# Performance work log

Measured on AMD Instinct MI355X. Metric: run time of the kernel, lower is better.

The kernel has to match this reference:

```python
import jax, jax.numpy as jnp
import numpy as np
import math

B, C, P = 4, 256, 4096
H = 4
EPS = 1e-5


def setup_inputs() -> dict:
    key = jax.random.key(0)
    ks = jax.random.split(key, 6)
    s = 1.0 / math.sqrt(C)
    return {
        "x": jax.random.normal(ks[0], (B, C, P), jnp.float32),
        "wq": jax.random.normal(ks[1], (C, C), jnp.float32) * s,
        "wk": jax.random.normal(ks[2], (C, C), jnp.float32) * s,
        "wv": jax.random.normal(ks[3], (C, C), jnp.float32) * s,
        "wt": jax.random.normal(ks[4], (C, C), jnp.float32) * s,
        "bt": jax.random.normal(ks[5], (C,), jnp.float32) * 0.01,
        "gamma": jnp.ones((C,), jnp.float32),
        "beta": jnp.zeros((C,), jnp.float32),
    }


def reference(x, wq, wk, wv, wt, bt, gamma, beta):
    b, c, p = x.shape
    d = c // H  # head dim
    # 1x1 Conv1d == channel matmul: [C_out, C_in] @ [B, C_in, P]
    q = jnp.einsum("oc,bcp->bop", wq, x).reshape(b, H, d, p)
    k = jnp.einsum("oc,bcp->bop", wk, x).reshape(b, H, d, p)
    v = jnp.einsum("oc,bcp->bop", wv, x).reshape(b, H, d, p)
    # scores: x_q [b,h,p,d] @ x_k [b,h,d,p] -> [b,h,p,p]
    scores = jnp.einsum("bhdi,bhdj->bhij", q, k) / jnp.sqrt(jnp.float32(d))
    attn = jax.nn.softmax(scores, axis=-1)
    # attn @ v^T: [b,h,p,p] @ [b,h,p,d] -> [b,h,p,d], then back to [b,c,p]
    o = jnp.einsum("bhij,bhdj->bhdi", attn, v).reshape(b, c, p)
    # trans_conv(o - x) + bias
    y = jnp.einsum("oc,bcp->bop", wt, o - x) + bt[None, :, None]
    # BatchNorm1d (training mode): per-channel stats over (batch, points), biased var
    mean = jnp.mean(y, axis=(0, 2), keepdims=True)
    var = jnp.mean(jnp.square(y - mean), axis=(0, 2), keepdims=True)
    y = (y - mean) * jax.lax.rsqrt(var + EPS)
    y = y * gamma[None, :, None] + beta[None, :, None]
    return x + jax.nn.relu(y)
```

## Files before the change

kernel.cpp:

```cpp
#include <hip/hip_runtime.h>
#include <stdint.h>

#define B_ 4
#define C_ 256
#define P_ 4096
#define H_ 4
#define EPS_ 1e-5f
#define LOG2E 1.4426950408889634f

typedef __attribute__((ext_vector_type(8))) short short8v;
typedef __attribute__((ext_vector_type(4))) float floatx4;
#define MFMA16 __builtin_amdgcn_mfma_f32_16x16x32_bf16

#define GLOAD16(gp, lp)                                                     \
  __builtin_amdgcn_global_load_lds(                                         \
      (const __attribute__((address_space(1))) uint32_t*)(gp),              \
      (__attribute__((address_space(3))) uint32_t*)(lp), 16, 0, 0)

#define EXP2IP(x) asm("v_exp_f32 %0, %0" : "+v"(x))

__device__ __forceinline__ ushort f2bf(float f) {
  union { float f; uint32_t u; } c; c.f = f;
  uint32_t r = c.u + 0x7FFFu + ((c.u >> 16) & 1u);
  return (ushort)(r >> 16);
}
__device__ __forceinline__ float bf2f(ushort u) {
  union { uint32_t u; float f; } c; c.u = ((uint32_t)u) << 16; return c.f;
}

__global__ __launch_bounds__(256) void cast_kernel(
    const float* __restrict__ x, ushort* __restrict__ xb) {
  const int p0 = blockIdx.x * 64;
  const int c0 = blockIdx.y * 64;
  const int b = blockIdx.z;
  __shared__ float Ls[64][69];
  const int t = threadIdx.x;
#pragma unroll
  for (int r = 0; r < 4; r++) {
    int g = t + r * 256;
    int c = g >> 4, p4 = (g & 15) * 4;
    *(float4*)&Ls[c][p4] =
        *(const float4*)&x[((size_t)(b * C_ + c0 + c)) * P_ + p0 + p4];
  }
  __syncthreads();
  const int p = t >> 2, cs = (t & 3) * 16;
  size_t rowb = ((size_t)b * P_ + p0 + p) * 256 + c0 + cs;
#pragma unroll
  for (int u = 0; u < 4; u++) {
    ushort4 o;
    o.x = f2bf(Ls[cs + u * 4 + 0][p]);
    o.y = f2bf(Ls[cs + u * 4 + 1][p]);
    o.z = f2bf(Ls[cs + u * 4 + 2][p]);
    o.w = f2bf(Ls[cs + u * 4 + 3][p]);
    *(ushort4*)&xb[rowb + u * 4] = o;
  }
}

__global__ __launch_bounds__(256) void proj_kernel(
    const ushort* __restrict__ xb, const float* __restrict__ wq,
    const float* __restrict__ wk, const float* __restrict__ wv,
    ushort* __restrict__ q, ushort* __restrict__ k, ushort* __restrict__ v) {
  const int p0 = blockIdx.x * 256;
  const int which = blockIdx.y >> 2;
  const int o0 = (blockIdx.y & 3) * 64;
  const int b = blockIdx.z;
  const float* __restrict__ w = (which == 0) ? wq : (which == 1) ? wk : wv;
  const float scale = (which == 0) ? 0.125f * LOG2E : 1.0f;

  __shared__ __align__(16) uint8_t smem[33280];
  ushort* As = (ushort*)smem;
  const int t = threadIdx.x;
  const int lane = t & 63, wid = t >> 6, lr = lane & 15, lg = lane >> 4;

#pragma unroll
  for (int r = 0; r < 8; r++) {
    int g = t + r * 256;
    int m = g >> 5, ch = g & 31;
    const float* wr = &w[(size_t)(o0 + m) * 256 + ch * 8];
    float4 wa = *(const float4*)wr, wb = *(const float4*)(wr + 4);
    short8v s;
    s[0] = f2bf(wa.x * scale); s[1] = f2bf(wa.y * scale);
    s[2] = f2bf(wa.z * scale); s[3] = f2bf(wa.w * scale);
    s[4] = f2bf(wb.x * scale); s[5] = f2bf(wb.y * scale);
    s[6] = f2bf(wb.z * scale); s[7] = f2bf(wb.w * scale);
    *(short8v*)&As[m * 256 + (ch ^ (m & 7)) * 8] = s;
  }
  __syncthreads();

  const int pw0 = p0 + wid * 64;
  floatx4 acc[4][4];
#pragma unroll
  for (int mt = 0; mt < 4; mt++)
#pragma unroll
    for (int pt = 0; pt < 4; pt++) acc[mt][pt] = (floatx4){0.f, 0.f, 0.f, 0.f};

#pragma unroll
  for (int ks = 0; ks < 4; ks++) {
    const int k0 = ks * 64;
    const int cb = k0 >> 3;
    short8v bf[4][2];
#pragma unroll
    for (int pt = 0; pt < 4; pt++)
#pragma unroll
      for (int kh = 0; kh < 2; kh++)
        bf[pt][kh] = *(const short8v*)&xb[((size_t)b * P_ + pw0 + pt * 16 + lr) * 256 +
                                          k0 + kh * 32 + lg * 8];
#pragma unroll
    for (int mt = 0; mt < 4; mt++) {
      int m = mt * 16 + lr;
      short8v a0 = *(const short8v*)&As[m * 256 + ((cb + lg) ^ (m & 7)) * 8];
      short8v a1 = *(const short8v*)&As[m * 256 + ((cb + 4 + lg) ^ (m & 7)) * 8];
#pragma unroll
      for (int pt = 0; pt < 4; pt++) {
        acc[mt][pt] = MFMA16(a0, bf[pt][0], acc[mt][pt], 0, 0, 0);
        acc[mt][pt] = MFMA16(a1, bf[pt][1], acc[mt][pt], 0, 0, 0);
      }
    }
  }

  if (which < 2) {
    ushort* out = (which == 0) ? q : k;
    const int h = o0 >> 6;
#pragma unroll
    for (int pt = 0; pt < 4; pt++) {
      size_t prow = ((size_t)(b * H_ + h) * P_ + pw0 + pt * 16 + lr) * 64;
#pragma unroll
      for (int mt = 0; mt < 4; mt++) {
        ushort4 s;
        s.x = f2bf(acc[mt][pt][0]); s.y = f2bf(acc[mt][pt][1]);
        s.z = f2bf(acc[mt][pt][2]); s.w = f2bf(acc[mt][pt][3]);
        *(ushort4*)&out[prow + mt * 16 + 4 * lg] = s;
      }
    }
  } else {
    __syncthreads();
    ushort* Vt = (ushort*)smem;
#pragma unroll
    for (int mt = 0; mt < 4; mt++)
#pragma unroll
      for (int rr = 0; rr < 4; rr++) {
        int c = mt * 16 + 4 * lg + rr;
#pragma unroll
        for (int pt = 0; pt < 4; pt++) {
          int s = 32 * (pt >> 1) + 8 * (lr >> 2) + 4 * (pt & 1) + (lr & 3);
          Vt[c * 260 + wid * 64 + s] = f2bf(acc[mt][pt][rr]);
        }
      }
    __syncthreads();
#pragma unroll
    for (int r = 0; r < 8; r++) {
      int g = t + r * 256;
      int cr = g >> 5, seg = g & 31;
      *(short8v*)&v[((size_t)(b * C_ + o0 + cr)) * P_ + p0 + seg * 8] =
          *(const short8v*)&Vt[cr * 260 + seg * 8];
    }
  }
}

__global__ __launch_bounds__(512, 4) void attn_kernel(
    const ushort* __restrict__ q, const ushort* __restrict__ k,
    const ushort* __restrict__ v, const ushort* __restrict__ xb,
    ushort* __restrict__ dmT) {
  const int i0 = blockIdx.x * 128;
  const int h = blockIdx.y;
  const int b = blockIdx.z;
  const int t = threadIdx.x;
  const int lane = t & 63, w = t >> 6, lr = lane & 15, lg = lane >> 4;
  const int qgrp = w & 3, jgrp = w >> 2;

  __shared__ __align__(16) uint8_t smem[65536];

  const size_t bh = (size_t)(b * H_ + h);
  const ushort* __restrict__ qg = q + bh * P_ * 64;
  const ushort* __restrict__ kb = k + bh * P_ * 64;
  const ushort* __restrict__ vb = v + ((size_t)(b * C_ + h * 64)) * P_;

  short8v bq0[2], bq1[2];
#pragma unroll
  for (int qb2 = 0; qb2 < 2; qb2++) {
    const ushort* qrow = qg + ((size_t)(i0 + qgrp * 32 + qb2 * 16 + lr)) * 64;
    bq0[qb2] = *(const short8v*)&qrow[lg * 8];
    bq1[qb2] = *(const short8v*)&qrow[32 + lg * 8];
  }

  short8v a_ones;
#pragma unroll
  for (int e = 0; e < 8; e++) a_ones[e] = (short)0x3F80;

  const int sw = lr & 7;
  const ushort* rb0 = (const ushort*)smem + jgrp * 16384 + lr * 64 + ((lg ^ sw) << 3);
  const ushort* rb1 = (const ushort*)smem + jgrp * 16384 + lr * 64 + (((4 + lg) ^ sw) << 3);

  const int rws = lane >> 3;
  const int srow = qgrp * 16 + rws;
  const int csw = ((lane & 7) ^ rws) * 8;
  const ushort* kg = kb + (size_t)srow * 64 + csw + (size_t)jgrp * 4096;
  const ushort* vg = vb + (size_t)srow * P_ + csw + jgrp * 64;
  ushort* kd0 = (ushort*)(smem + jgrp * 32768) + qgrp * 1024;

  floatx4 o_acc[2][4], lacc[2];
#pragma unroll
  for (int qb2 = 0; qb2 < 2; qb2++) {
    lacc[qb2] = (floatx4){0.f, 0.f, 0.f, 0.f};
#pragma unroll
    for (int dt = 0; dt < 4; dt++) o_acc[qb2][dt] = (floatx4){0.f, 0.f, 0.f, 0.f};
  }

#define STAGE_(SEL)                                                         \
  do {                                                                      \
    ushort* _kd = kd0 + (SEL) * 8192;                                       \
    GLOAD16(kg, _kd);                                                       \
    GLOAD16(kg + 512, _kd + 512);                                           \
    GLOAD16(vg, _kd + 4096);                                                \
    GLOAD16(vg + 8 * (size_t)P_, _kd + 4608);                               \
    kg += 8192;                                                             \
    vg += 128;                                                              \
  } while (0)

#define COMPUTE_(SEL)                                                       \
  do {                                                                      \
    floatx4 st[2][4];                                                       \
    _Pragma("unroll") for (int jt = 0; jt < 4; jt++) {                      \
      short8v a0 = *(const short8v*)&rb0[(SEL) * 8192 + jt * 1024];         \
      short8v a1 = *(const short8v*)&rb1[(SEL) * 8192 + jt * 1024];         \
      floatx4 c0 = (floatx4){0.f, 0.f, 0.f, 0.f};                           \
      c0 = MFMA16(a0, bq0[0], c0, 0, 0, 0);                                 \
      c0 = MFMA16(a1, bq1[0], c0, 0, 0, 0);                                 \
      st[0][jt] = c0;                                                       \
      floatx4 c1 = (floatx4){0.f, 0.f, 0.f, 0.f};                           \
      c1 = MFMA16(a0, bq0[1], c1, 0, 0, 0);                                 \
      c1 = MFMA16(a1, bq1[1], c1, 0, 0, 0);                                 \
      st[1][jt] = c1;                                                       \
    }                                                                       \
    short8v bp0[2], bp1[2];                                                 \
    _Pragma("unroll") for (int qb2 = 0; qb2 < 2; qb2++) {                   \
      _Pragma("unroll") for (int jt = 0; jt < 4; jt++) {                    \
        EXP2IP(st[qb2][jt][0]); EXP2IP(st[qb2][jt][1]);                     \
        EXP2IP(st[qb2][jt][2]); EXP2IP(st[qb2][jt][3]);                     \
      }                                                                     \
      union { short8v v8; uint32_t d[4]; } u0, u1;                          \
      asm("v_cvt_pk_bf16_f32 %0, %1, %2" : "=v"(u0.d[0]) : "v"(st[qb2][0][0]), "v"(st[qb2][0][1])); \
      asm("v_cvt_pk_bf16_f32 %0, %1, %2" : "=v"(u0.d[1]) : "v"(st[qb2][0][2]), "v"(st[qb2][0][3])); \
      asm("v_cvt_pk_bf16_f32 %0, %1, %2" : "=v"(u0.d[2]) : "v"(st[qb2][1][0]), "v"(st[qb2][1][1])); \
      asm("v_cvt_pk_bf16_f32 %0, %1, %2" : "=v"(u0.d[3]) : "v"(st[qb2][1][2]), "v"(st[qb2][1][3])); \
      asm("v_cvt_pk_bf16_f32 %0, %1, %2" : "=v"(u1.d[0]) : "v"(st[qb2][2][0]), "v"(st[qb2][2][1])); \
      asm("v_cvt_pk_bf16_f32 %0, %1, %2" : "=v"(u1.d[1]) : "v"(st[qb2][2][2]), "v"(st[qb2][2][3])); \
      asm("v_cvt_pk_bf16_f32 %0, %1, %2" : "=v"(u1.d[2]) : "v"(st[qb2][3][0]), "v"(st[qb2][3][1])); \
      asm("v_cvt_pk_bf16_f32 %0, %1, %2" : "=v"(u1.d[3]) : "v"(st[qb2][3][2]), "v"(st[qb2][3][3])); \
      bp0[qb2] = u0.v8;                                                     \
      bp1[qb2] = u1.v8;                                                     \
    }                                                                       \
    _Pragma("unroll") for (int dt = 0; dt < 4; dt++) {                      \
      short8v a0 = *(const short8v*)&rb0[(SEL) * 8192 + 4096 + dt * 1024];  \
      short8v a1 = *(const short8v*)&rb1[(SEL) * 8192 + 4096 + dt * 1024];  \
      o_acc[0][dt] = MFMA16(a0, bp0[0], o_acc[0][dt], 0, 0, 0);             \
      o_acc[0][dt] = MFMA16(a1, bp1[0], o_acc[0][dt], 0, 0, 0);             \
      o_acc[1][dt] = MFMA16(a0, bp0[1], o_acc[1][dt], 0, 0, 0);             \
      o_acc[1][dt] = MFMA16(a1, bp1[1], o_acc[1][dt], 0, 0, 0);             \
    }                                                                       \
    lacc[0] = MFMA16(a_ones, bp0[0], lacc[0], 0, 0, 0);                     \
    lacc[0] = MFMA16(a_ones, bp1[0], lacc[0], 0, 0, 0);                     \
    lacc[1] = MFMA16(a_ones, bp0[1], lacc[1], 0, 0, 0);                     \
    lacc[1] = MFMA16(a_ones, bp1[1], lacc[1], 0, 0, 0);                     \
  } while (0)

  STAGE_(0);
  for (int it = 0; it < 15; ++it) {
    STAGE_(1);
    asm volatile("s_waitcnt vmcnt(4)" ::: "memory");
    __builtin_amdgcn_s_barrier();
    COMPUTE_(0);
    asm volatile("" ::: "memory");
    __builtin_amdgcn_s_barrier();
    STAGE_(0);
    asm volatile("s_waitcnt vmcnt(4)" ::: "memory");
    __builtin_amdgcn_s_barrier();
    COMPUTE_(1);
    asm volatile("" ::: "memory");
    __builtin_amdgcn_s_barrier();
  }
  STAGE_(1);
  asm volatile("s_waitcnt vmcnt(4)" ::: "memory");
  __builtin_amdgcn_s_barrier();
  COMPUTE_(0);
  asm volatile("s_waitcnt vmcnt(0)" ::: "memory");
  __builtin_amdgcn_s_barrier();
  COMPUTE_(1);
  __syncthreads();
#undef STAGE_
#undef COMPUTE_

  float* Opart = (float*)smem;
  float* lpart = (float*)(smem + 32768);
  if (jgrp == 1) {
#pragma unroll
    for (int qb2 = 0; qb2 < 2; qb2++) {
#pragma unroll
      for (int dt = 0; dt < 4; dt++)
        *(floatx4*)&Opart[(((qgrp * 2 + qb2) * 4 + dt) << 8) + (lane << 2)] =
            o_acc[qb2][dt];
      if (lg == 0) lpart[qgrp * 32 + qb2 * 16 + lr] = lacc[qb2][0];
    }
  }
  __syncthreads();
  ushort* Os = (ushort*)(smem + 36864);
  if (jgrp == 0) {
#pragma unroll
    for (int qb2 = 0; qb2 < 2; qb2++) {
      const int i = qgrp * 32 + qb2 * 16 + lr;
      const float invl = 1.f / (lacc[qb2][0] + lpart[i]);
#pragma unroll
      for (int dt = 0; dt < 4; dt++) {
        floatx4 o2 = o_acc[qb2][dt] +
                     *(const floatx4*)&Opart[(((qgrp * 2 + qb2) * 4 + dt) << 8) + (lane << 2)];
        uint2 pk2;
        asm("v_cvt_pk_bf16_f32 %0, %1, %2" : "=v"(pk2.x)
            : "v"(o2[0] * invl), "v"(o2[1] * invl));
        asm("v_cvt_pk_bf16_f32 %0, %1, %2" : "=v"(pk2.y)
            : "v"(o2[2] * invl), "v"(o2[3] * invl));
        *(uint2*)&Os[i * 72 + dt * 16 + 4 * lg] = pk2;
      }
    }
  }
  __syncthreads();
  const int ei = t >> 2, edq = t & 3;
  size_t rowb = ((size_t)b * P_ + i0 + ei) * 256 + h * 64 + edq * 16;
#pragma unroll
  for (int u = 0; u < 2; u++) {
    short8v xv8 = *(const short8v*)&xb[rowb + u * 8];
    short8v ov8 = *(const short8v*)&Os[ei * 72 + edq * 16 + u * 8];
    short8v res;
#pragma unroll
    for (int e = 0; e < 8; e++) {
      float d = bf2f(((const ushort*)&ov8)[e]) - bf2f(((const ushort*)&xv8)[e]);
      ((ushort*)&res)[e] = f2bf(d);
    }
    *(short8v*)&dmT[rowb + u * 8] = res;
  }
}

__global__ __launch_bounds__(256) void tconv_kernel(
    const ushort* __restrict__ dmT, const float* __restrict__ wt,
    const float* __restrict__ bt, ushort* __restrict__ y) {
  const int p0 = blockIdx.x * 128;
  const int o0 = blockIdx.y * 64;
  const int b = blockIdx.z;
  __shared__ __align__(16) uint8_t smem[32768];
  ushort* As = (ushort*)smem;
  const int t = threadIdx.x;
  const int lane = t & 63, wid = t >> 6, lr = lane & 15, lg = lane >> 4;

#pragma unroll
  for (int r = 0; r < 8; r++) {
    int g = t + r * 256;
    int m = g >> 5, ch = g & 31;
    const float* wr = &wt[(size_t)(o0 + m) * 256 + ch * 8];
    float4 wa = *(const float4*)wr, wb = *(const float4*)(wr + 4);
    short8v s;
    s[0] = f2bf(wa.x); s[1] = f2bf(wa.y); s[2] = f2bf(wa.z); s[3] = f2bf(wa.w);
    s[4] = f2bf(wb.x); s[5] = f2bf(wb.y); s[6] = f2bf(wb.z); s[7] = f2bf(wb.w);
    *(short8v*)&As[m * 256 + (ch ^ (m & 7)) * 8] = s;
  }
  __syncthreads();

  const int pw0 = p0 + wid * 32;
  floatx4 acc[4][2];
#pragma unroll
  for (int mt = 0; mt < 4; mt++)
#pragma unroll
    for (int pt = 0; pt < 2; pt++) acc[mt][pt] = (floatx4){0.f, 0.f, 0.f, 0.f};

#pragma unroll
  for (int ks = 0; ks < 4; ks++) {
    const int k0 = ks * 64;
    const int cb = k0 >> 3;
    short8v bf[2][2];
#pragma unroll
    for (int pt = 0; pt < 2; pt++)
#pragma unroll
      for (int kh = 0; kh < 2; kh++)
        bf[pt][kh] = *(const short8v*)&dmT[((size_t)b * P_ + pw0 + pt * 16 + lr) * 256 +
                                           k0 + kh * 32 + lg * 8];
#pragma unroll
    for (int mt = 0; mt < 4; mt++) {
      int m = mt * 16 + lr;
      short8v a0 = *(const short8v*)&As[m * 256 + ((cb + lg) ^ (m & 7)) * 8];
      short8v a1 = *(const short8v*)&As[m * 256 + ((cb + 4 + lg) ^ (m & 7)) * 8];
#pragma unroll
      for (int pt = 0; pt < 2; pt++) {
        acc[mt][pt] = MFMA16(a0, bf[pt][0], acc[mt][pt], 0, 0, 0);
        acc[mt][pt] = MFMA16(a1, bf[pt][1], acc[mt][pt], 0, 0, 0);
      }
    }
  }

  __syncthreads();
  ushort* Yt = (ushort*)smem;
#pragma unroll
  for (int mt = 0; mt < 4; mt++) {
    float4 bv = *(const float4*)&bt[o0 + mt * 16 + 4 * lg];
#pragma unroll
    for (int rr = 0; rr < 4; rr++) {
      float bias = (rr == 0) ? bv.x : (rr == 1) ? bv.y : (rr == 2) ? bv.z : bv.w;
      int c = mt * 16 + 4 * lg + rr;
#pragma unroll
      for (int pt = 0; pt < 2; pt++)
        Yt[c * 132 + wid * 32 + pt * 16 + lr] = f2bf(acc[mt][pt][rr] + bias);
    }
  }
  __syncthreads();
#pragma unroll
  for (int r = 0; r < 4; r++) {
    int g = t + r * 256;
    int cr = g >> 4, seg = g & 15;
    *(short8v*)&y[((size_t)(b * C_ + o0 + cr)) * P_ + p0 + seg * 8] =
        *(const short8v*)&Yt[cr * 132 + seg * 8];
  }
}

__global__ __launch_bounds__(256) void bnstats_kernel(
    const ushort* __restrict__ y, const float* __restrict__ gamma,
    const float* __restrict__ beta, float* __restrict__ sc,
    float* __restrict__ sh) {
  const int c = blockIdx.x;
  const int t = threadIdx.x;
  float s1 = 0.f, s2 = 0.f;
#pragma unroll
  for (int r = 0; r < 8; r++) {
    int e = t + r * 256;
    int b = e >> 9;
    int p8 = (e & 511) * 8;
    short8v yv = *(const short8v*)&y[((size_t)(b * C_ + c)) * P_ + p8];
#pragma unroll
    for (int j = 0; j < 8; j++) {
      float f = bf2f(((const ushort*)&yv)[j]);
      s1 += f; s2 += f * f;
    }
  }
#pragma unroll
  for (int off = 32; off > 0; off >>= 1) {
    s1 += __shfl_xor(s1, off);
    s2 += __shfl_xor(s2, off);
  }
  __shared__ float r1[4], r2[4];
  const int w = t >> 6;
  if ((t & 63) == 0) { r1[w] = s1; r2[w] = s2; }
  __syncthreads();
  if (t == 0) {
    float a1 = r1[0] + r1[1] + r1[2] + r1[3];
    float a2 = r2[0] + r2[1] + r2[2] + r2[3];
    const float n = (float)(B_ * P_);
    float mean = a1 / n;
    float var = a2 / n - mean * mean;
    float rstd = rsqrtf(var + EPS_);
    float g = gamma[c] * rstd;
    sc[c] = g;
    sh[c] = beta[c] - mean * g;
  }
}

__global__ __launch_bounds__(256) void final_kernel(
    const float* __restrict__ x, const ushort* __restrict__ y,
    const float* __restrict__ sc, const float* __restrict__ sh,
    float* __restrict__ out) {
  const int f = blockIdx.x * 256 + threadIdx.x;
  const size_t base = (size_t)f * 8;
  const int c = (int)((base >> 12) & (C_ - 1));
  short8v yv = *(const short8v*)&y[base];
  float4 x0 = *(const float4*)&x[base];
  float4 x1 = *(const float4*)&x[base + 4];
  const float s = sc[c], hh = sh[c];
  float4 r0, r1;
  r0.x = x0.x + fmaxf(bf2f(((const ushort*)&yv)[0]) * s + hh, 0.f);
  r0.y = x0.y + fmaxf(bf2f(((const ushort*)&yv)[1]) * s + hh, 0.f);
  r0.z = x0.z + fmaxf(bf2f(((const ushort*)&yv)[2]) * s + hh, 0.f);
  r0.w = x0.w + fmaxf(bf2f(((const ushort*)&yv)[3]) * s + hh, 0.f);
  r1.x = x1.x + fmaxf(bf2f(((const ushort*)&yv)[4]) * s + hh, 0.f);
  r1.y = x1.y + fmaxf(bf2f(((const ushort*)&yv)[5]) * s + hh, 0.f);
  r1.z = x1.z + fmaxf(bf2f(((const ushort*)&yv)[6]) * s + hh, 0.f);
  r1.w = x1.w + fmaxf(bf2f(((const ushort*)&yv)[7]) * s + hh, 0.f);
  *(float4*)&out[base] = r0;
  *(float4*)&out[base + 4] = r1;
}

extern "C" void kernel_launch(void* const* d_in, const int* in_sizes, int n_in,
                              void* d_out, int out_size, void* d_ws, size_t ws_size,
                              hipStream_t stream) {
  const float* x = (const float*)d_in[0];
  const float* wq = (const float*)d_in[1];
  const float* wk = (const float*)d_in[2];
  const float* wv = (const float*)d_in[3];
  const float* wt = (const float*)d_in[4];
  const float* bt = (const float*)d_in[5];
  const float* gamma = (const float*)d_in[6];
  const float* beta = (const float*)d_in[7];
  float* out = (float*)d_out;
  char* wsb = (char*)d_ws;

  const size_t N = (size_t)B_ * C_ * P_;
  ushort* xb = (ushort*)wsb;
  ushort* q = (ushort*)(wsb + N * 2);
  ushort* k = (ushort*)(wsb + N * 4);
  ushort* v = (ushort*)(wsb + N * 6);
  ushort* dmT = (ushort*)(wsb + N * 8);
  ushort* y = (ushort*)(wsb + N * 10);
  float* sc = (float*)wsb;
  float* sh = sc + C_;

  cast_kernel<<<dim3(P_ / 64, C_ / 64, B_), 256, 0, stream>>>(x, xb);
  proj_kernel<<<dim3(P_ / 256, 12, B_), 256, 0, stream>>>(xb, wq, wk, wv, q, k, v);
  attn_kernel<<<dim3(P_ / 128, H_, B_), 512, 0, stream>>>(q, k, v, xb, dmT);
  tconv_kernel<<<dim3(P_ / 128, 4, B_), 256, 0, stream>>>(dmT, wt, bt, y);
  bnstats_kernel<<<C_, 256, 0, stream>>>(y, gamma, beta, sc, sh);
  final_kernel<<<(int)(N / 8 / 256), 256, 0, stream>>>(x, y, sc, sh, out);
}
```

Measured before the change: 121.5 us.

## Fuse BatchNorm statistics into tconv epilogue via atomics and relax attention waitcnt

Result: slower. 137.7 us (+13.3%).

```diff
diff --git a/kernel.cpp b/kernel.cpp
--- a/kernel.cpp
+++ b/kernel.cpp
@@ -267,20 +267,20 @@
   STAGE_(0);
   for (int it = 0; it < 15; ++it) {
     STAGE_(1);
-    asm volatile("s_waitcnt vmcnt(4)" ::: "memory");
+    asm volatile("s_waitcnt vmcnt(8)" ::: "memory");
     __builtin_amdgcn_s_barrier();
     COMPUTE_(0);
     asm volatile("" ::: "memory");
     __builtin_amdgcn_s_barrier();
     STAGE_(0);
-    asm volatile("s_waitcnt vmcnt(4)" ::: "memory");
+    asm volatile("s_waitcnt vmcnt(8)" ::: "memory");
     __builtin_amdgcn_s_barrier();
     COMPUTE_(1);
     asm volatile("" ::: "memory");
     __builtin_amdgcn_s_barrier();
   }
   STAGE_(1);
-  asm volatile("s_waitcnt vmcnt(4)" ::: "memory");
+  asm volatile("s_waitcnt vmcnt(8)" ::: "memory");
   __builtin_amdgcn_s_barrier();
   COMPUTE_(0);
   asm volatile("s_waitcnt vmcnt(0)" ::: "memory");
@@ -341,7 +341,8 @@
 
 __global__ __launch_bounds__(256) void tconv_kernel(
     const ushort* __restrict__ dmT, const float* __restrict__ wt,
-    const float* __restrict__ bt, ushort* __restrict__ y) {
+    const float* __restrict__ bt, ushort* __restrict__ y,
+    float* __restrict__ gs1, float* __restrict__ gs2) {
   const int p0 = blockIdx.x * 128;
   const int o0 = blockIdx.y * 64;
   const int b = blockIdx.z;
@@ -413,50 +414,38 @@
   for (int r = 0; r < 4; r++) {
     int g = t + r * 256;
     int cr = g >> 4, seg = g & 15;
-    *(short8v*)&y[((size_t)(b * C_ + o0 + cr)) * P_ + p0 + seg * 8] =
-        *(const short8v*)&Yt[cr * 132 + seg * 8];
-  }
-}
-
-__global__ __launch_bounds__(256) void bnstats_kernel(
-    const ushort* __restrict__ y, const float* __restrict__ gamma,
-    const float* __restrict__ beta, float* __restrict__ sc,
-    float* __restrict__ sh) {
-  const int c = blockIdx.x;
-  const int t = threadIdx.x;
-  float s1 = 0.f, s2 = 0.f;
-#pragma unroll
-  for (int r = 0; r < 8; r++) {
-    int e = t + r * 256;
-    int b = e >> 9;
-    int p8 = (e & 511) * 8;
-    short8v yv = *(const short8v*)&y[((size_t)(b * C_ + c)) * P_ + p8];
-#pragma unroll
-    for (int j = 0; j < 8; j++) {
-      float f = bf2f(((const ushort*)&yv)[j]);
+    short8v yv8 = *(const short8v*)&Yt[cr * 132 + seg * 8];
+    *(short8v*)&y[((size_t)(b * C_ + o0 + cr)) * P_ + p0 + seg * 8] = yv8;
+    float s1 = 0.f, s2 = 0.f;
+#pragma unroll
+    for (int e = 0; e < 8; e++) {
+      float f = bf2f(((const ushort*)&yv8)[e]);
       s1 += f; s2 += f * f;
     }
-  }
-#pragma unroll
-  for (int off = 32; off > 0; off >>= 1) {
-    s1 += __shfl_xor(s1, off);
-    s2 += __shfl_xor(s2, off);
-  }
-  __shared__ float r1[4], r2[4];
-  const int w = t >> 6;
-  if ((t & 63) == 0) { r1[w] = s1; r2[w] = s2; }
-  __syncthreads();
-  if (t == 0) {
-    float a1 = r1[0] + r1[1] + r1[2] + r1[3];
-    float a2 = r2[0] + r2[1] + r2[2] + r2[3];
-    const float n = (float)(B_ * P_);
-    float mean = a1 / n;
-    float var = a2 / n - mean * mean;
-    float rstd = rsqrtf(var + EPS_);
-    float g = gamma[c] * rstd;
-    sc[c] = g;
-    sh[c] = beta[c] - mean * g;
-  }
+#pragma unroll
+    for (int off = 1; off <= 8; off <<= 1) {
+      s1 += __shfl_xor(s1, off);
+      s2 += __shfl_xor(s2, off);
+    }
+    if ((t & 15) == 0) {
+      atomicAdd(&gs1[o0 + cr], s1);
+      atomicAdd(&gs2[o0 + cr], s2);
+    }
+  }
+}
+
+__global__ __launch_bounds__(256) void bnfinal_kernel(
+    const float* __restrict__ gs1, const float* __restrict__ gs2,
+    const float* __restrict__ gamma, const float* __restrict__ beta,
+    float* __restrict__ sc, float* __restrict__ sh) {
+  const int c = threadIdx.x;
+  const float n = (float)(B_ * P_);
+  float mean = gs1[c] / n;
+  float var = gs2[c] / n - mean * mean;
+  float rstd = rsqrtf(var + EPS_);
+  float g = gamma[c] * rstd;
+  sc[c] = g;
+  sh[c] = beta[c] - mean * g;
 }
 
 __global__ __launch_bounds__(256) void final_kernel(
@@ -504,13 +493,16 @@
   ushort* v = (ushort*)(wsb + N * 6);
   ushort* dmT = (ushort*)(wsb + N * 8);
   ushort* y = (ushort*)(wsb + N * 10);
+  float* gs1 = (float*)(wsb + N * 12);
+  float* gs2 = gs1 + C_;
   float* sc = (float*)wsb;
   float* sh = sc + C_;
 
+  hipMemsetAsync(gs1, 0, 2 * C_ * sizeof(float), stream);
   cast_kernel<<<dim3(P_ / 64, C_ / 64, B_), 256, 0, stream>>>(x, xb);
   proj_kernel<<<dim3(P_ / 256, 12, B_), 256, 0, stream>>>(xb, wq, wk, wv, q, k, v);
   attn_kernel<<<dim3(P_ / 128, H_, B_), 512, 0, stream>>>(q, k, v, xb, dmT);
-  tconv_kernel<<<dim3(P_ / 128, 4, B_), 256, 0, stream>>>(dmT, wt, bt, y);
-  bnstats_kernel<<<C_, 256, 0, stream>>>(y, gamma, beta, sc, sh);
+  tconv_kernel<<<dim3(P_ / 128, 4, B_), 256, 0, stream>>>(dmT, wt, bt, y, gs1, gs2);
+  bnfinal_kernel<<<1, 256, 0, stream>>>(gs1, gs2, gamma, beta, sc, sh);
   final_kernel<<<(int)(N / 8 / 256), 256, 0, stream>>>(x, y, sc, sh, out);
 }
```
